# Kernel optimization log

Hardware: AMD Instinct MI355X
Metric: run time of the kernel (lower is better)

## Reference

```python
import jax, jax.numpy as jnp
import numpy as np

NR = 116  # number of AAL ROIs
VOL = (61, 73, 61)
V = 61 * 73 * 61


def setup_inputs() -> dict:
    B, C, D, T = 8, 192, 2, 24  # batch MUST be 8: fc1 outputs 64 = B*B
    key = jax.random.key(0)
    ks = jax.random.split(key, 16)
    s = 0.02
    # synthetic AAL template: every voxel gets a ROI label 0..115, all present
    rng = np.random.default_rng(0)
    labels_np = rng.integers(0, NR, size=V).astype(np.int32)
    labels_np[:NR] = np.arange(NR)
    # ROI centroid pairwise distances (compute_node_distances equivalent)
    coords = np.stack(np.meshgrid(np.arange(61), np.arange(73), np.arange(61), indexing='ij'), -1).reshape(V, 3).astype(np.float64)
    cent = np.zeros((NR, 3))
    for r in range(NR):
        cent[r] = coords[labels_np == r].mean(0)
    dist = np.linalg.norm(cent[:, None] - cent[None, :], axis=-1).astype(np.float32)
    return {
        'x': jax.random.normal(ks[0], (B, C, D, D, D, T), jnp.float32),
        'roi_labels': jnp.asarray(labels_np.reshape(VOL)),
        'node_distances': jnp.asarray(dist),
        'fc_w': s * jax.random.normal(ks[1], (V, C * D * D * D), jnp.float32),
        'fc_b': jnp.zeros((V,), jnp.float32),
        'fs_w1': s * jax.random.normal(ks[2], (NR, 64), jnp.float32),
        'fs_b1': jnp.zeros((NR, 64), jnp.float32),
        'fs_w2': s * jax.random.normal(ks[3], (NR, 64, 64), jnp.float32),
        'fs_b2': jnp.zeros((NR, 64), jnp.float32),
        'fs_w3': s * jax.random.normal(ks[4], (NR, 64), jnp.float32),
        'fs_b3': jnp.zeros((NR,), jnp.float32),
        'm_w1': s * jax.random.normal(ks[5], (64,), jnp.float32),
        'm_b1': jnp.zeros((64,), jnp.float32),
        'm_w2': s * jax.random.normal(ks[6], (64, 64), jnp.float32),
        'm_b2': jnp.zeros((64,), jnp.float32),
        'm_w3': s * jax.random.normal(ks[7], (64,), jnp.float32),
        'm_b3': jnp.zeros((1,), jnp.float32),
        'fc1_w': s * jax.random.normal(ks[8], (64, NR * NR), jnp.float32),
        'fc1_b': jnp.zeros((64,), jnp.float32),
        'hidden_w': s * jax.random.normal(ks[9], (768, 192 + NR), jnp.float32),
        'hidden_b': jnp.zeros((768,), jnp.float32),
        'out_w': s * jax.random.normal(ks[10], (1, 768), jnp.float32),
        'out_b': jnp.zeros((1,), jnp.float32),
    }


def _forward(x, node_distances, fc_w, fc_b, fs_w1, fs_b1, fs_w2, fs_b2, fs_w3, fs_b3,
             m_w1, m_b1, m_w2, m_b2, m_w3, m_b3, fc1_w, fc1_b,
             hidden_w, hidden_b, out_w, out_b, labels):
    B, T = x.shape[0], x.shape[-1]
    # fc projects each time frame into the 61x73x61 volume: [B,T,V]
    xt = jnp.swapaxes(x.reshape(B, -1, T), 1, 2)            # [B,T,1536]
    vox = jnp.einsum('bti,vi->btv', xt, fc_w) + fc_b        # [B,T,V]
    # ROI time series = segment-mean of voxels per ROI (replaces python loops)
    seg = jax.ops.segment_sum(jnp.moveaxis(vox, 2, 0).reshape(V, B * T), labels, num_segments=NR)
    cnt = jax.ops.segment_sum(jnp.ones((V,), vox.dtype), labels, num_segments=NR)
    ts = (seg / jnp.maximum(cnt, 1.0)[:, None]).reshape(NR, B, T)
    x_node = ts.mean(axis=2).T                              # [B,116]
    # 116 tiny per-ROI MLPs, vectorized (eval mode: dropout is identity)
    h = jax.nn.relu(x_node[..., None] * fs_w1[None] + fs_b1[None])       # [B,116,64]
    h = jax.nn.relu(jnp.einsum('bni,noi->bno', h, fs_w2) + fs_b2[None])  # [B,116,64]
    fx = jnp.einsum('bni,ni->bn', h, fs_w3) + fs_b3[None]                # [B,116]
    # distance MLP m over all 116*116 pairwise distances
    d = node_distances.reshape(-1, 1)                       # [13456,1]
    g = jax.nn.relu(d * m_w1[None, :] + m_b1)
    g = jax.nn.relu(g @ m_w2.T + m_b2)
    md = (g @ m_w3[:, None] + m_b3).reshape(-1)             # [13456]
    mmat = (fc1_w @ md + fc1_b).reshape(B, B)               # requires B*B == 64
    mf = mmat @ fx                                          # [B,116]
    # avgpool branch: mean over all spatial*time positions -> [B,192]
    pooled = x.reshape(B, x.shape[1], -1).mean(axis=2)
    cat = jnp.concatenate([mf, pooled], axis=1)             # [B,308]
    hid = cat @ hidden_w.T + hidden_b                       # no activation (as in source)
    return hid @ out_w.T + out_b                            # [B,1]


def reference(x, roi_labels, node_distances, fc_w, fc_b, fs_w1, fs_b1, fs_w2, fs_b2, fs_w3, fs_b3,
              m_w1, m_b1, m_w2, m_b2, m_w3, m_b3, fc1_w, fc1_b, hidden_w, hidden_b, out_w, out_b):
    return _forward(x, node_distances, fc_w, fc_b, fs_w1, fs_b1, fs_w2, fs_b2, fs_w3, fs_b3,
                    m_w1, m_b1, m_w2, m_b2, m_w3, m_b3, fc1_w, fc1_b,
                    hidden_w, hidden_b, out_w, out_b, roi_labels.reshape(-1))
```

## Files before the change

kernel.cpp:

```cpp
#include <hip/hip_runtime.h>

#define V_TOT 271633
#define NRR 116
#define CIN 1536
#define T_LEN 24
#define B_SZ 8
#define NP (NRR*NRR)
#define CATN 308
#define SPLITS 44
#define VB 1062
#define WPAD 310
#define DPS 12

typedef float nfloat4 __attribute__((ext_vector_type(4)));

__global__ __launch_bounds__(256) void hist_xbar_kernel(const int* __restrict__ labels,
                                                        int* __restrict__ blockHist,
                                                        const float* __restrict__ x,
                                                        float* __restrict__ xbar) {
    if (blockIdx.x < VB) {
        __shared__ int h[NRR];
        for (int i = threadIdx.x; i < NRR; i += 256) h[i] = 0;
        __syncthreads();
        int v = blockIdx.x * 256 + threadIdx.x;
        if (v < V_TOT) atomicAdd(&h[labels[v]], 1);
        __syncthreads();
        for (int i = threadIdx.x; i < NRR; i += 256)
            blockHist[(size_t)i * VB + blockIdx.x] = h[i];
    } else {
        int idx = (blockIdx.x - VB) * 256 + threadIdx.x;
        if (idx < B_SZ * CIN) {
            const float* p = x + (size_t)idx * T_LEN;
            float s = 0.f;
            #pragma unroll
            for (int t = 0; t < T_LEN; ++t) s += p[t];
            xbar[idx] = s * (1.0f / T_LEN);
        }
    }
}

__global__ __launch_bounds__(256) void binscan_kernel(const int* __restrict__ blockHist,
                                                      int* __restrict__ blockBase,
                                                      int* __restrict__ counts) {
    const int r = blockIdx.x;
    const int lane = threadIdx.x & 63, w = threadIdx.x >> 6;
    __shared__ int wsum[4];
    int run = 0;
    for (int base = 0; base < VB; base += 256) {
        const int i = base + threadIdx.x;
        const int orig = (i < VB) ? blockHist[(size_t)r * VB + i] : 0;
        int val = orig;
        #pragma unroll
        for (int off = 1; off < 64; off <<= 1) {
            int t = __shfl_up(val, off);
            if (lane >= off) val += t;
        }
        if (lane == 63) wsum[w] = val;
        __syncthreads();
        int woff = 0;
        #pragma unroll
        for (int j = 0; j < 4; ++j) if (j < w) woff += wsum[j];
        if (i < VB) blockBase[(size_t)r * VB + i] = run + woff + val - orig;
        int tot = wsum[0] + wsum[1] + wsum[2] + wsum[3];
        __syncthreads();
        run += tot;
    }
    if (threadIdx.x == 0) counts[r] = run;
}

__global__ void offsets_kernel(const int* __restrict__ counts, int* __restrict__ offsets) {
    if (threadIdx.x == 0) {
        int acc = 0;
        for (int r = 0; r < NRR; ++r) { offsets[r] = acc; acc += counts[r]; }
        offsets[NRR] = acc;
    }
}

__global__ __launch_bounds__(256) void scatter_kernel(const int* __restrict__ labels,
                                                      const int* __restrict__ offsets,
                                                      const int* __restrict__ blockBase,
                                                      int* __restrict__ perm) {
    __shared__ int lab[256];
    const int v = blockIdx.x * 256 + threadIdx.x;
    const int r = (v < V_TOT) ? labels[v] : -1;
    lab[threadIdx.x] = r;
    __syncthreads();
    if (r >= 0) {
        int rank = 0;
        for (int t = 0; t < (int)threadIdx.x; ++t) rank += (lab[t] == r);
        perm[offsets[r] + blockBase[(size_t)r * VB + blockIdx.x] + rank] = v;
    }
}

__device__ __forceinline__ void add4(float4& a, const float4 b) {
    a.x += b.x; a.y += b.y; a.z += b.z; a.w += b.w;
}
__device__ __forceinline__ float4 ldnt4(const float* p) {
    nfloat4 v = __builtin_nontemporal_load((const nfloat4*)p);
    return make_float4(v.x, v.y, v.z, v.w);
}

__global__ __launch_bounds__(384, 6) void roi_partial_dot_kernel(
        const float* __restrict__ fc_w, const float* __restrict__ fc_b,
        const int* __restrict__ perm,
        const int* __restrict__ counts, const int* __restrict__ offsets,
        const float* __restrict__ xbar, float* __restrict__ dotpart) {
    const int r = blockIdx.x, s = blockIdx.y;
    const int n = counts[r], off = offsets[r];
    const int chunk = (n + SPLITS - 1) / SPLITS;
    const int k0 = min(s * chunk, n);
    const int k1 = min(k0 + chunk, n);
    const int c4 = threadIdx.x * 4;

    float4 a0{0,0,0,0}, a1{0,0,0,0}, a2{0,0,0,0}, a3{0,0,0,0};
    float4 a4{0,0,0,0}, a5{0,0,0,0}, a6{0,0,0,0}, a7{0,0,0,0};
    int k = k0;
    for (; k + 8 <= k1; k += 8) {
        const int v0 = perm[off+k+0], v1 = perm[off+k+1], v2 = perm[off+k+2], v3 = perm[off+k+3];
        const int v4 = perm[off+k+4], v5 = perm[off+k+5], v6 = perm[off+k+6], v7 = perm[off+k+7];
        const float4 x0 = ldnt4(fc_w + (size_t)v0*CIN + c4);
        const float4 x1 = ldnt4(fc_w + (size_t)v1*CIN + c4);
        const float4 x2 = ldnt4(fc_w + (size_t)v2*CIN + c4);
        const float4 x3 = ldnt4(fc_w + (size_t)v3*CIN + c4);
        const float4 x4 = ldnt4(fc_w + (size_t)v4*CIN + c4);
        const float4 x5 = ldnt4(fc_w + (size_t)v5*CIN + c4);
        const float4 x6 = ldnt4(fc_w + (size_t)v6*CIN + c4);
        const float4 x7 = ldnt4(fc_w + (size_t)v7*CIN + c4);
        add4(a0, x0); add4(a1, x1); add4(a2, x2); add4(a3, x3);
        add4(a4, x4); add4(a5, x5); add4(a6, x6); add4(a7, x7);
    }
    for (; k < k1; ++k) {
        const int v = perm[off+k];
        add4(a0, ldnt4(fc_w + (size_t)v*CIN + c4));
    }
    add4(a0, a1); add4(a2, a3); add4(a4, a5); add4(a6, a7);
    add4(a0, a2); add4(a4, a6); add4(a0, a4);

    float bacc = 0.f;
    for (int kk = k0 + threadIdx.x; kk < k1; kk += 384) bacc += fc_b[perm[off+kk]];

    float d[B_SZ];
    #pragma unroll
    for (int b = 0; b < B_SZ; ++b) {
        const float4 xb = *(const float4*)(xbar + b*CIN + c4);
        d[b] = a0.x*xb.x + a0.y*xb.y + a0.z*xb.z + a0.w*xb.w;
    }
    __shared__ float red[6][9];
    const int lane = threadIdx.x & 63, w = threadIdx.x >> 6;
    #pragma unroll
    for (int b = 0; b < B_SZ; ++b) {
        float v = d[b];
        for (int sft = 32; sft > 0; sft >>= 1) v += __shfl_down(v, sft);
        if (lane == 0) red[w][b] = v;
    }
    {
        float v = bacc;
        for (int sft = 32; sft > 0; sft >>= 1) v += __shfl_down(v, sft);
        if (lane == 0) red[w][8] = v;
    }
    __syncthreads();
    if (threadIdx.x < 9) {
        float v = 0.f;
        #pragma unroll
        for (int j = 0; j < 6; ++j) v += red[j][threadIdx.x];
        dotpart[((size_t)(r*SPLITS + s))*DPS + threadIdx.x] = v;
    }
}

__global__ void fs_mlp_kernel(const float* __restrict__ dotpart, const int* __restrict__ counts,
                              const float* __restrict__ w1, const float* __restrict__ b1,
                              const float* __restrict__ w2, const float* __restrict__ b2,
                              const float* __restrict__ w3, const float* __restrict__ b3,
                              float* __restrict__ fx) {
    int w = blockIdx.x * 4 + (threadIdx.x >> 6);
    int lane = threadIdx.x & 63;
    int b = w / NRR, r = w % NRR;
    float sdot = 0.f, sb = 0.f;
    if (lane < SPLITS) {
        const float* p = dotpart + ((size_t)(r*SPLITS + lane))*DPS;
        sdot = p[b]; sb = p[8];
    }
    #pragma unroll
    for (int off = 32; off > 0; off >>= 1) {
        sdot += __shfl_xor(sdot, off);
        sb   += __shfl_xor(sb, off);
    }
    float xn = (sdot + sb) / (float)counts[r];

    float h1 = fmaxf(xn * w1[r*64 + lane] + b1[r*64 + lane], 0.f);
    const float* w2row = w2 + ((size_t)r*64 + lane) * 64;
    float acc = b2[r*64 + lane];
    #pragma unroll
    for (int i = 0; i < 64; ++i) acc += __shfl(h1, i) * w2row[i];
    float h2 = fmaxf(acc, 0.f);
    float p = h2 * w3[r*64 + lane];
    for (int sft = 32; sft > 0; sft >>= 1) p += __shfl_down(p, sft);
    if (lane == 0) fx[b * NRR + r] = p + b3[r];
}

__global__ void dist_mlp_kernel(const float* __restrict__ dist,
                                const float* __restrict__ mw1, const float* __restrict__ mb1,
                                const float* __restrict__ mw2, const float* __restrict__ mb2,
                                const float* __restrict__ mw3, const float* __restrict__ mb3,
                                float* __restrict__ md) {
    int p = blockIdx.x * 4 + (threadIdx.x >> 6);
    int lane = threadIdx.x & 63;
    float d = dist[p];
    float g1 = fmaxf(d * mw1[lane] + mb1[lane], 0.f);
    const float* w2row = mw2 + lane * 64;
    float acc = mb2[lane];
    #pragma unroll
    for (int i = 0; i < 64; ++i) acc += __shfl(g1, i) * w2row[i];
    float g2 = fmaxf(acc, 0.f);
    float t = g2 * mw3[lane];
    for (int s = 32; s > 0; s >>= 1) t += __shfl_down(t, s);
    if (lane == 0) md[p] = t + mb3[0];
}

__global__ __launch_bounds__(256) void fc1_kernel(const float* __restrict__ fc1_w,
                                                  const float* __restrict__ md,
                                                  float* __restrict__ mmatpart) {
    const int j = blockIdx.x, q = blockIdx.y;
    const int p0 = q * (NP/4), p1 = p0 + (NP/4);
    const float* row = fc1_w + (size_t)j * NP;
    float s = 0.f;
    for (int p = p0 + threadIdx.x; p < p1; p += 256) s += row[p] * md[p];
    __shared__ float red[4];
    for (int sft = 32; sft > 0; sft >>= 1) s += __shfl_down(s, sft);
    if ((threadIdx.x & 63) == 0) red[threadIdx.x >> 6] = s;
    __syncthreads();
    if (threadIdx.x == 0) mmatpart[j*4 + q] = red[0] + red[1] + red[2] + red[3];
}

__global__ __launch_bounds__(256) void weff_kernel(const float* __restrict__ hidden_w,
                                                   const float* __restrict__ hidden_b,
                                                   const float* __restrict__ out_w,
                                                   const float* __restrict__ out_b,
                                                   float* __restrict__ weffpart) {
    const int k = blockIdx.x * 256 + threadIdx.x;
    const int jb = blockIdx.y;
    const int j0 = jb * 96, j1 = j0 + 96;
    if (k < CATN) {
        float s = 0.f;
        for (int j = j0; j < j1; ++j) s += hidden_w[(size_t)j * CATN + k] * out_w[j];
        weffpart[jb*WPAD + k] = s;
    } else if (k == CATN) {
        float s = 0.f;
        for (int j = j0; j < j1; ++j) s += hidden_b[j] * out_w[j];
        weffpart[jb*WPAD + CATN] = s + (jb == 0 ? out_b[0] : 0.f);
    }
}

__global__ __launch_bounds__(512) void tail_kernel(const float* __restrict__ mmatpart,
                                                   const float* __restrict__ fc1_b,
                                                   const float* __restrict__ fx,
                                                   const float* __restrict__ xbar,
                                                   const float* __restrict__ weffpart,
                                                   float* __restrict__ out) {
    __shared__ float mmat[64];
    __shared__ float cat[B_SZ][CATN];
    if (threadIdx.x < 64) {
        const float* p = mmatpart + threadIdx.x*4;
        mmat[threadIdx.x] = p[0] + p[1] + p[2] + p[3] + fc1_b[threadIdx.x];
    }
    __syncthreads();
    for (int idx = threadIdx.x; idx < B_SZ * NRR; idx += 512) {
        int b = idx / NRR, r = idx % NRR;
        float s = 0.f;
        #pragma unroll
        for (int kk = 0; kk < 8; ++kk) s += mmat[b*8 + kk] * fx[kk * NRR + r];
        cat[b][r] = s;
    }
    for (int idx = threadIdx.x; idx < B_SZ * 192; idx += 512) {
        int b = idx / 192, c = idx % 192;
        float s = 0.f;
        #pragma unroll
        for (int j = 0; j < 8; ++j) s += xbar[b * CIN + c*8 + j];
        cat[b][NRR + c] = s * (1.0f / 8.0f);
    }
    __syncthreads();
    const int b = threadIdx.x >> 6, lane = threadIdx.x & 63;
    float s = 0.f;
    for (int k = lane; k < CATN; k += 64) {
        float wk = 0.f;
        #pragma unroll
        for (int jb = 0; jb < 8; ++jb) wk += weffpart[jb*WPAD + k];
        s += cat[b][k] * wk;
    }
    for (int sft = 32; sft > 0; sft >>= 1) s += __shfl_down(s, sft);
    if (lane == 0) {
        float beff = 0.f;
        #pragma unroll
        for (int jb = 0; jb < 8; ++jb) beff += weffpart[jb*WPAD + CATN];
        out[b] = s + beff;
    }
}

extern "C" void kernel_launch(void* const* d_in, const int* in_sizes, int n_in,
                              void* d_out, int out_size, void* d_ws, size_t ws_size,
                              hipStream_t stream) {
    const float* x        = (const float*)d_in[0];
    const int*   labels   = (const int*)d_in[1];
    const float* dist     = (const float*)d_in[2];
    const float* fc_w     = (const float*)d_in[3];
    const float* fc_b     = (const float*)d_in[4];
    const float* fs_w1    = (const float*)d_in[5];
    const float* fs_b1    = (const float*)d_in[6];
    const float* fs_w2    = (const float*)d_in[7];
    const float* fs_b2    = (const float*)d_in[8];
    const float* fs_w3    = (const float*)d_in[9];
    const float* fs_b3    = (const float*)d_in[10];
    const float* m_w1     = (const float*)d_in[11];
    const float* m_b1     = (const float*)d_in[12];
    const float* m_w2     = (const float*)d_in[13];
    const float* m_b2     = (const float*)d_in[14];
    const float* m_w3     = (const float*)d_in[15];
    const float* m_b3     = (const float*)d_in[16];
    const float* fc1_w    = (const float*)d_in[17];
    const float* fc1_b    = (const float*)d_in[18];
    const float* hidden_w = (const float*)d_in[19];
    const float* hidden_b = (const float*)d_in[20];
    const float* out_w    = (const float*)d_in[21];
    const float* out_b    = (const float*)d_in[22];
    float* out = (float*)d_out;

    int* counts    = (int*)d_ws;
    int* offsets   = counts + 128;
    int* blockHist = offsets + 128;
    int* blockBase = blockHist + NRR*VB;
    int* perm      = blockBase + NRR*VB;
    float* fb = (float*)(perm + ((V_TOT + 255) / 256) * 256);
    float* dotpart  = fb;  fb += (size_t)NRR * SPLITS * DPS;
    float* xbar     = fb;  fb += B_SZ * CIN;
    float* fx       = fb;  fb += B_SZ * NRR + 32;
    float* md       = fb;  fb += NP;
    float* mmatpart = fb;  fb += 256;
    float* weffpart = fb;  fb += 8 * WPAD;

    hist_xbar_kernel<<<VB + 48, 256, 0, stream>>>(labels, blockHist, x, xbar);
    binscan_kernel<<<NRR, 256, 0, stream>>>(blockHist, blockBase, counts);
    offsets_kernel<<<1, 64, 0, stream>>>(counts, offsets);
    scatter_kernel<<<VB, 256, 0, stream>>>(labels, offsets, blockBase, perm);
    roi_partial_dot_kernel<<<dim3(NRR, SPLITS), 384, 0, stream>>>(fc_w, fc_b, perm, counts, offsets, xbar, dotpart);
    dist_mlp_kernel<<<NP / 4, 256, 0, stream>>>(dist, m_w1, m_b1, m_w2, m_b2, m_w3, m_b3, md);
    fc1_kernel<<<dim3(64, 4), 256, 0, stream>>>(fc1_w, md, mmatpart);
    weff_kernel<<<dim3(2, 8), 256, 0, stream>>>(hidden_w, hidden_b, out_w, out_b, weffpart);
    fs_mlp_kernel<<<232, 256, 0, stream>>>(dotpart, counts, fs_w1, fs_b1, fs_w2, fs_b2, fs_w3, fs_b3, fx);
    tail_kernel<<<1, 512, 0, stream>>>(mmatpart, fc1_b, fx, xbar, weffpart, out);
}
```

Measured before the change: 348.8 us.

## Merge independent stages into block-partitioned mega and mid kernels

```diff
diff --git a/kernel.cpp b/kernel.cpp
--- a/kernel.cpp
+++ b/kernel.cpp
@@ -8,9 +8,12 @@
 #define NP (NRR*NRR)
 #define CATN 308
 #define SPLITS 44
+#define NST (NRR*SPLITS)
 #define VB 1062
 #define WPAD 310
 #define DPS 12
+#define DISTB 2243
+#define MEGA_STREAM_BASE (DISTB + 8)
 
 typedef float nfloat4 __attribute__((ext_vector_type(4)));
 
@@ -100,12 +103,56 @@
     return make_float4(v.x, v.y, v.z, v.w);
 }
 
-__global__ __launch_bounds__(384, 6) void roi_partial_dot_kernel(
+__global__ __launch_bounds__(384, 6) void mega_kernel(
         const float* __restrict__ fc_w, const float* __restrict__ fc_b,
         const int* __restrict__ perm,
         const int* __restrict__ counts, const int* __restrict__ offsets,
-        const float* __restrict__ xbar, float* __restrict__ dotpart) {
-    const int r = blockIdx.x, s = blockIdx.y;
+        const float* __restrict__ xbar, float* __restrict__ dotpart,
+        const float* __restrict__ dist,
+        const float* __restrict__ mw1, const float* __restrict__ mb1,
+        const float* __restrict__ mw2, const float* __restrict__ mb2,
+        const float* __restrict__ mw3, const float* __restrict__ mb3,
+        float* __restrict__ md,
+        const float* __restrict__ hidden_w, const float* __restrict__ hidden_b,
+        const float* __restrict__ out_w, const float* __restrict__ out_b,
+        float* __restrict__ weffpart) {
+    const int bid = blockIdx.x;
+    const int lane = threadIdx.x & 63, w = threadIdx.x >> 6;
+
+    if (bid < DISTB) {
+        const int p = bid * 6 + w;
+        if (p < NP) {
+            float d = dist[p];
+            float g1 = fmaxf(d * mw1[lane] + mb1[lane], 0.f);
+            const float* w2row = mw2 + lane * 64;
+            float acc = mb2[lane];
+            #pragma unroll
+            for (int i = 0; i < 64; ++i) acc += __shfl(g1, i) * w2row[i];
+            float g2 = fmaxf(acc, 0.f);
+            float t = g2 * mw3[lane];
+            for (int s = 32; s > 0; s >>= 1) t += __shfl_down(t, s);
+            if (lane == 0) md[p] = t + mb3[0];
+        }
+        return;
+    }
+    if (bid < MEGA_STREAM_BASE) {
+        const int jb = bid - DISTB;
+        const int k = threadIdx.x;
+        const int j0 = jb * 96, j1 = j0 + 96;
+        if (k < CATN) {
+            float s = 0.f;
+            for (int j = j0; j < j1; ++j) s += hidden_w[(size_t)j * CATN + k] * out_w[j];
+            weffpart[jb*WPAD + k] = s;
+        } else if (k == CATN) {
+            float s = 0.f;
+            for (int j = j0; j < j1; ++j) s += hidden_b[j] * out_w[j];
+            weffpart[jb*WPAD + CATN] = s + (jb == 0 ? out_b[0] : 0.f);
+        }
+        return;
+    }
+
+    const int sbid = bid - MEGA_STREAM_BASE;
+    const int r = sbid / SPLITS, s = sbid % SPLITS;
     const int n = counts[r], off = offsets[r];
     const int chunk = (n + SPLITS - 1) / SPLITS;
     const int k0 = min(s * chunk, n);
@@ -146,7 +193,6 @@
         d[b] = a0.x*xb.x + a0.y*xb.y + a0.z*xb.z + a0.w*xb.w;
     }
     __shared__ float red[6][9];
-    const int lane = threadIdx.x & 63, w = threadIdx.x >> 6;
     #pragma unroll
     for (int b = 0; b < B_SZ; ++b) {
         float v = d[b];
@@ -167,87 +213,52 @@
     }
 }
 
-__global__ void fs_mlp_kernel(const float* __restrict__ dotpart, const int* __restrict__ counts,
-                              const float* __restrict__ w1, const float* __restrict__ b1,
-                              const float* __restrict__ w2, const float* __restrict__ b2,
-                              const float* __restrict__ w3, const float* __restrict__ b3,
-                              float* __restrict__ fx) {
-    int w = blockIdx.x * 4 + (threadIdx.x >> 6);
-    int lane = threadIdx.x & 63;
-    int b = w / NRR, r = w % NRR;
-    float sdot = 0.f, sb = 0.f;
-    if (lane < SPLITS) {
-        const float* p = dotpart + ((size_t)(r*SPLITS + lane))*DPS;
-        sdot = p[b]; sb = p[8];
-    }
-    #pragma unroll
-    for (int off = 32; off > 0; off >>= 1) {
-        sdot += __shfl_xor(sdot, off);
-        sb   += __shfl_xor(sb, off);
-    }
-    float xn = (sdot + sb) / (float)counts[r];
-
-    float h1 = fmaxf(xn * w1[r*64 + lane] + b1[r*64 + lane], 0.f);
-    const float* w2row = w2 + ((size_t)r*64 + lane) * 64;
-    float acc = b2[r*64 + lane];
-    #pragma unroll
-    for (int i = 0; i < 64; ++i) acc += __shfl(h1, i) * w2row[i];
-    float h2 = fmaxf(acc, 0.f);
-    float p = h2 * w3[r*64 + lane];
-    for (int sft = 32; sft > 0; sft >>= 1) p += __shfl_down(p, sft);
-    if (lane == 0) fx[b * NRR + r] = p + b3[r];
-}
-
-__global__ void dist_mlp_kernel(const float* __restrict__ dist,
-                                const float* __restrict__ mw1, const float* __restrict__ mb1,
-                                const float* __restrict__ mw2, const float* __restrict__ mb2,
-                                const float* __restrict__ mw3, const float* __restrict__ mb3,
-                                float* __restrict__ md) {
-    int p = blockIdx.x * 4 + (threadIdx.x >> 6);
-    int lane = threadIdx.x & 63;
-    float d = dist[p];
-    float g1 = fmaxf(d * mw1[lane] + mb1[lane], 0.f);
-    const float* w2row = mw2 + lane * 64;
-    float acc = mb2[lane];
-    #pragma unroll
-    for (int i = 0; i < 64; ++i) acc += __shfl(g1, i) * w2row[i];
-    float g2 = fmaxf(acc, 0.f);
-    float t = g2 * mw3[lane];
-    for (int s = 32; s > 0; s >>= 1) t += __shfl_down(t, s);
-    if (lane == 0) md[p] = t + mb3[0];
-}
-
-__global__ __launch_bounds__(256) void fc1_kernel(const float* __restrict__ fc1_w,
-                                                  const float* __restrict__ md,
-                                                  float* __restrict__ mmatpart) {
-    const int j = blockIdx.x, q = blockIdx.y;
-    const int p0 = q * (NP/4), p1 = p0 + (NP/4);
-    const float* row = fc1_w + (size_t)j * NP;
-    float s = 0.f;
-    for (int p = p0 + threadIdx.x; p < p1; p += 256) s += row[p] * md[p];
-    __shared__ float red[4];
-    for (int sft = 32; sft > 0; sft >>= 1) s += __shfl_down(s, sft);
-    if ((threadIdx.x & 63) == 0) red[threadIdx.x >> 6] = s;
-    __syncthreads();
-    if (threadIdx.x == 0) mmatpart[j*4 + q] = red[0] + red[1] + red[2] + red[3];
-}
-
-__global__ __launch_bounds__(256) void weff_kernel(const float* __restrict__ hidden_w,
-                                                   const float* __restrict__ hidden_b,
-                                                   const float* __restrict__ out_w,
-                                                   const float* __restrict__ out_b,
-                                                   float* __restrict__ weffpart) {
-    const int k = blockIdx.x * 256 + threadIdx.x;
-    const int jb = blockIdx.y;
-    const int j0 = jb * 96, j1 = j0 + 96;
-    if (k < CATN) {
+__global__ __launch_bounds__(256) void mid_kernel(
+        const float* __restrict__ dotpart, const int* __restrict__ counts,
+        const float* __restrict__ w1, const float* __restrict__ b1,
+        const float* __restrict__ w2, const float* __restrict__ b2,
+        const float* __restrict__ w3, const float* __restrict__ b3,
+        float* __restrict__ fx,
+        const float* __restrict__ fc1_w, const float* __restrict__ md,
+        float* __restrict__ mmatpart) {
+    const int bid = blockIdx.x;
+    const int lane = threadIdx.x & 63;
+    if (bid < 232) {
+        int w = bid * 4 + (threadIdx.x >> 6);
+        int b = w / NRR, r = w % NRR;
+        float sdot = 0.f, sb = 0.f;
+        if (lane < SPLITS) {
+            const float* p = dotpart + ((size_t)(r*SPLITS + lane))*DPS;
+            sdot = p[b]; sb = p[8];
+        }
+        #pragma unroll
+        for (int off = 32; off > 0; off >>= 1) {
+            sdot += __shfl_xor(sdot, off);
+            sb   += __shfl_xor(sb, off);
+        }
+        float xn = (sdot + sb) / (float)counts[r];
+
+        float h1 = fmaxf(xn * w1[r*64 + lane] + b1[r*64 + lane], 0.f);
+        const float* w2row = w2 + ((size_t)r*64 + lane) * 64;
+        float acc = b2[r*64 + lane];
+        #pragma unroll
+        for (int i = 0; i < 64; ++i) acc += __shfl(h1, i) * w2row[i];
+        float h2 = fmaxf(acc, 0.f);
+        float p = h2 * w3[r*64 + lane];
+        for (int sft = 32; sft > 0; sft >>= 1) p += __shfl_down(p, sft);
+        if (lane == 0) fx[b * NRR + r] = p + b3[r];
+    } else {
+        const int fb = bid - 232;
+        const int j = fb >> 2, q = fb & 3;
+        const int p0 = q * (NP/4), p1 = p0 + (NP/4);
+        const float* row = fc1_w + (size_t)j * NP;
         float s = 0.f;
-        for (int j = j0; j < j1; ++j) s += hidden_w[(size_t)j * CATN + k] * out_w[j];
-        weffpart[jb*WPAD + k] = s;
-    } else if (k == CATN) {
-        float s = 0.f;
-        for (int j = j0; j < j1; ++j) s += hidden_b[j] * out_w[j];
-        weffpart[jb*WPAD + CATN] = s + (jb == 0 ? out_b[0] : 0.f);
+        for (int p = p0 + threadIdx.x; p < p1; p += 256) s += row[p] * md[p];
+        __shared__ float red[4];
+        for (int sft = 32; sft > 0; sft >>= 1) s += __shfl_down(s, sft);
+        if ((threadIdx.x & 63) == 0) red[threadIdx.x >> 6] = s;
+        __syncthreads();
+        if (threadIdx.x == 0) mmatpart[j*4 + q] = red[0] + red[1] + red[2] + red[3];
     }
 }
 
@@ -341,10 +352,11 @@
     binscan_kernel<<<NRR, 256, 0, stream>>>(blockHist, blockBase, counts);
     offsets_kernel<<<1, 64, 0, stream>>>(counts, offsets);
     scatter_kernel<<<VB, 256, 0, stream>>>(labels, offsets, blockBase, perm);
-    roi_partial_dot_kernel<<<dim3(NRR, SPLITS), 384, 0, stream>>>(fc_w, fc_b, perm, counts, offsets, xbar, dotpart);
-    dist_mlp_kernel<<<NP / 4, 256, 0, stream>>>(dist, m_w1, m_b1, m_w2, m_b2, m_w3, m_b3, md);
-    fc1_kernel<<<dim3(64, 4), 256, 0, stream>>>(fc1_w, md, mmatpart);
-    weff_kernel<<<dim3(2, 8), 256, 0, stream>>>(hidden_w, hidden_b, out_w, out_b, weffpart);
-    fs_mlp_kernel<<<232, 256, 0, stream>>>(dotpart, counts, fs_w1, fs_b1, fs_w2, fs_b2, fs_w3, fs_b3, fx);
+    mega_kernel<<<MEGA_STREAM_BASE + NST, 384, 0, stream>>>(
+        fc_w, fc_b, perm, counts, offsets, xbar, dotpart,
+        dist, m_w1, m_b1, m_w2, m_b2, m_w3, m_b3, md,
+        hidden_w, hidden_b, out_w, out_b, weffpart);
+    mid_kernel<<<488, 256, 0, stream>>>(dotpart, counts,
+        fs_w1, fs_b1, fs_w2, fs_b2, fs_w3, fs_b3, fx, fc1_w, md, mmatpart);
     tail_kernel<<<1, 512, 0, stream>>>(mmatpart, fc1_b, fx, xbar, weffpart, out);
 }
```

Measured after the change: 324.5 us. 1.07x faster.
